# Kernel optimization log

Hardware: AMD Instinct MI355X
Metric: run time of the kernel (lower is better)

## Reference

```python
import jax, jax.numpy as jnp
import numpy as np

L, B, E = 512, 32, 512
ENC_HID, DEC_HID = 512, 1024
H2 = 2 * ENC_HID            # bidirectional encoder output dim
OUT_DIM = 32000             # generation (trg) vocab
CPY_LEN = 60000             # copy vocab size (embedding rows / prediction cols)
SRC_V = 50000
NEG = -1e10


def setup_inputs() -> dict:
    key = jax.random.key(0)
    ks = jax.random.split(key, 20)
    s = 0.02
    f32 = jnp.float32
    return {
        "src": jax.random.randint(ks[0], (L, B), 0, SRC_V),
        "inp": jax.random.randint(ks[1], (B,), 0, CPY_LEN),
        "hidden": jax.random.normal(ks[2], (2, B, DEC_HID), f32),
        "c": jax.random.normal(ks[3], (2, B, DEC_HID), f32),
        "encoder_outputs": jax.random.normal(ks[4], (L, B, H2), f32),
        "mask": jnp.ones((B, L), jnp.int32),
        "selective_weights": jax.random.normal(ks[5], (B, L - 2), f32),
        "src_to_cpy": jax.random.randint(ks[6], (SRC_V,), 0, CPY_LEN),
        # learned parameters
        "emb": jax.random.normal(ks[7], (CPY_LEN, E), f32) * s,
        "W_attn": jax.random.normal(ks[8], (H2 + DEC_HID, DEC_HID), f32) * s,
        "b_attn": jnp.zeros((DEC_HID,), f32),
        "v_attn": jax.random.normal(ks[9], (DEC_HID,), f32) * s,
        "W_ih0": jax.random.normal(ks[10], (4 * DEC_HID, 2 * H2 + E), f32) * s,
        "W_hh0": jax.random.normal(ks[11], (4 * DEC_HID, DEC_HID), f32) * s,
        "b_ih0": jnp.zeros((4 * DEC_HID,), f32),
        "b_hh0": jnp.zeros((4 * DEC_HID,), f32),
        "W_ih1": jax.random.normal(ks[12], (4 * DEC_HID, DEC_HID), f32) * s,
        "W_hh1": jax.random.normal(ks[13], (4 * DEC_HID, DEC_HID), f32) * s,
        "b_ih1": jnp.zeros((4 * DEC_HID,), f32),
        "b_hh1": jnp.zeros((4 * DEC_HID,), f32),
        "W_fc": jax.random.normal(ks[14], (OUT_DIM, H2 + DEC_HID + E), f32) * s,
        "b_fc": jnp.zeros((OUT_DIM,), f32),
        "W_copy": jax.random.normal(ks[15], (DEC_HID, H2), f32) * s,
        "b_copy": jnp.zeros((DEC_HID,), f32),
    }


def _lstm_cell(x, h, c, W_ih, W_hh, b_ih, b_hh):
    # PyTorch gate order: i, f, g, o
    g = x @ W_ih.T + h @ W_hh.T + b_ih + b_hh
    i, f, gg, o = jnp.split(g, 4, axis=-1)
    c_new = jax.nn.sigmoid(f) * c + jax.nn.sigmoid(i) * jnp.tanh(gg)
    h_new = jax.nn.sigmoid(o) * jnp.tanh(c_new)
    return h_new, c_new


def reference(src, inp, hidden, c, encoder_outputs, mask, selective_weights,
              src_to_cpy, emb, W_attn, b_attn, v_attn,
              W_ih0, W_hh0, b_ih0, b_hh0, W_ih1, W_hh1, b_ih1, b_hh1,
              W_fc, b_fc, W_copy, b_copy):
    Bn = encoder_outputs.shape[1]
    Ln = encoder_outputs.shape[0]
    # update_selective_weights: mask where converted src token != prev prediction, softmax
    conv_src = src_to_cpy[src[1:-1]]              # [L-2, B]
    copy_mask = (conv_src == inp[None, :]).T      # [B, L-2]
    sel = jnp.where(copy_mask, selective_weights, NEG)
    sel = jax.nn.softmax(sel, axis=1)             # [B, L-2]
    embedded = emb[inp]                           # [B, E] (dropout in eval mode = identity)
    enc = jnp.transpose(encoder_outputs, (1, 0, 2))  # [B, L, H2]
    # Bahdanau attention over encoder outputs
    h_top = hidden[-1]                            # [B, D]
    h_rep = jnp.broadcast_to(h_top[:, None, :], (Bn, Ln, h_top.shape[-1]))
    energy = jnp.tanh(jnp.concatenate([h_rep, enc], axis=2) @ W_attn + b_attn)  # [B, L, D]
    scores = energy @ v_attn                      # [B, L]
    scores = jnp.where(mask == 0, NEG, scores)
    attn_w = jax.nn.softmax(scores, axis=1)
    attentive_read = jnp.einsum('bl,blh->bh', attn_w, enc)        # [B, H2]
    sel = jnp.where(mask[:, 1:-1] == 0, NEG, sel)                 # faithful second mask
    selective_read = jnp.einsum('bl,blh->bh', sel, enc[:, 1:-1])  # [B, H2]
    # 2-layer LSTM, single step
    x = jnp.concatenate([embedded, attentive_read, selective_read], axis=1)
    h0, c0 = _lstm_cell(x, hidden[0], c[0], W_ih0, W_hh0, b_ih0, b_hh0)
    h1, c1 = _lstm_cell(h0, hidden[1], c[1], W_ih1, W_hh1, b_ih1, b_hh1)
    hidden_new = jnp.stack([h0, h1])
    c_new = jnp.stack([c0, c1])
    # generation scores
    gen = jnp.concatenate([h1, attentive_read, embedded], axis=1) @ W_fc.T + b_fc  # [B, OUT_DIM]
    # copy scores over trimmed source positions
    proj = jnp.tanh(enc[:, 1:-1] @ W_copy.T + b_copy)             # [B, L-2, D]
    copy_scores = jnp.einsum('bld,bd->bl', proj, h1)              # [B, L-2]
    copy_scores = jnp.where(mask[:, 1:-1] == 0, NEG, copy_scores)
    # assemble predictions: generation slice + indexed scatter of copy scores
    src_cpy = src_to_cpy[src.T[:, 1:-1]]                          # [B, L-2]
    preds = jnp.zeros((Bn, CPY_LEN), gen.dtype)
    preds = preds.at[:, :OUT_DIM].set(gen)
    preds = preds.at[jnp.arange(Bn)[:, None], src_cpy].set(copy_scores)
    return preds, hidden_new, c_new, attn_w, copy_scores
```

## Files before the change

### kernel.cpp

```cpp
#include <hip/hip_runtime.h>
#include <stdint.h>

typedef unsigned short u16;
typedef unsigned int   u32;
typedef __attribute__((ext_vector_type(8))) short short8;
typedef __attribute__((ext_vector_type(4))) float f32x4;

#define NEGF (-1.0e10f)

static constexpr int LL = 512, BB = 32, EE = 512, H2 = 1024, DH = 1024;
static constexpr int KX = 2560, OUTD = 32000, CPY = 60000;

static constexpr size_t HID_OFF   = 1920000;
static constexpr size_t C_OFF     = HID_OFF + 65536;
static constexpr size_t ATTN_OFF  = C_OFF + 65536;
static constexpr size_t CS_OFF    = ATTN_OFF + 16384;

static constexpr size_t WS_ENC    = 0;
static constexpr size_t WS_WA1T   = 33554432;
static constexpr size_t WS_WA2T   = 35651584;
static constexpr size_t WS_WCT    = 37748736;
static constexpr size_t WS_HPF    = 39845888;
static constexpr size_t WS_SCORES = 39976960;
static constexpr size_t WS_SELP   = 40108032;
static constexpr size_t WS_XBF    = 40173568;
static constexpr size_t WS_GENBF  = 40337408;
static constexpr size_t WS_H0PBF  = 40501248;
static constexpr size_t WS_H1PBF  = 40566784;
static constexpr size_t WS_H0NBF  = 40632320;
static constexpr size_t WS_PROJ   = 50331648;
static constexpr size_t WS_TOTAL  = WS_PROJ + 33554432;
static constexpr size_t WS_GPART  = WS_WA1T;
static constexpr size_t WS_TAG    = WS_ENC;

__device__ __forceinline__ u16 f2bf(float x){
  u32 u = __builtin_bit_cast(u32, x);
  u32 r = (u + 0x7FFFu + ((u >> 16) & 1u)) >> 16;
  return (u16)r;
}
__device__ __forceinline__ float bf2f(u16 h){
  u32 u = ((u32)h) << 16; return __builtin_bit_cast(float, u);
}
__device__ __forceinline__ float fsig(float x){ return 1.f/(1.f + __expf(-x)); }
__device__ __forceinline__ float ftanh(float x){
  float e = __expf(2.f*x);
  return 1.f - 2.f/(e + 1.f);
}

#define GLDS16(gp, lp) __builtin_amdgcn_global_load_lds( \
    (__attribute__((address_space(1))) void*)(gp), \
    (__attribute__((address_space(3))) void*)(lp), 16, 0, 0)

__global__ void k_f32_to_bf16(const float* __restrict__ in, u16* __restrict__ out, int n4){
  int stride = gridDim.x * blockDim.x;
  for (int i = blockIdx.x*blockDim.x + threadIdx.x; i < n4; i += stride){
    float4 v = ((const float4*)in)[i];
    u32 lo = (u32)f2bf(v.x) | ((u32)f2bf(v.y) << 16);
    u32 hi = (u32)f2bf(v.z) | ((u32)f2bf(v.w) << 16);
    ((uint2*)out)[i] = make_uint2(lo, hi);
  }
}

__global__ void k_wattn_t(const float* __restrict__ W, u16* __restrict__ wa1t, u16* __restrict__ wa2t){
  __shared__ float Tt[64*65];
  int n0 = blockIdx.x*64, k0 = blockIdx.y*64;
  int t = threadIdx.x;
  int nn = t & 63, kq = t >> 6;
  for (int kk = kq; kk < 64; kk += 4)
    Tt[kk*65 + nn] = W[(size_t)(k0+kk)*1024 + n0 + nn];
  __syncthreads();
  u16* dst = (k0 < 1024) ? wa1t : wa2t;
  int kbase = (k0 < 1024) ? k0 : (k0 - 1024);
  int kk2 = t & 63, nq = t >> 6;
  for (int nn2 = nq; nn2 < 64; nn2 += 4)
    dst[(size_t)(n0+nn2)*1024 + kbase + kk2] = f2bf(Tt[kk2*65 + nn2]);
}

__global__ void k_prep(const int* __restrict__ src, const int* __restrict__ inp,
                       const float* __restrict__ hidden, const float* __restrict__ selw,
                       const int* __restrict__ s2c, const float* __restrict__ emb,
                       const int* __restrict__ mask,
                       u16* __restrict__ xbf, u16* __restrict__ genbf,
                       u16* __restrict__ h0pbf, u16* __restrict__ h1pbf,
                       float* __restrict__ scores, float* __restrict__ selp)
{
  int b = blockIdx.x, t = threadIdx.x;
  int ib = inp[b];
  for (int h = t; h < 512; h += 256){
    u16 e = f2bf(emb[(size_t)ib*512 + h]);
    xbf[b*2560 + h] = e;
    genbf[b*2560 + 2048 + h] = e;
  }
  for (int k = t; k < 1024; k += 256){
    h0pbf[b*1024 + k] = f2bf(hidden[b*1024 + k]);
    h1pbf[b*1024 + k] = f2bf(hidden[32768 + b*1024 + k]);
  }
  for (int l = t; l < 512; l += 256)
    scores[b*512 + l] = 0.f;
  __shared__ float red[256];
  float lg[2];
  #pragma unroll
  for (int i = 0; i < 2; ++i){
    int j = t + i*256;
    lg[i] = NEGF;
    if (j < 510){
      int cs = s2c[src[(j+1)*32 + b]];
      if (cs == ib) lg[i] = selw[b*510 + j];
    }
  }
  red[t] = fmaxf(lg[0], lg[1]); __syncthreads();
  for (int s = 128; s > 0; s >>= 1){ if (t < s) red[t] = fmaxf(red[t], red[t+s]); __syncthreads(); }
  float mx = red[0]; __syncthreads();
  float e0 = (t < 510)     ? __expf(lg[0] - mx) : 0.f;
  float e1 = (t+256 < 510) ? __expf(lg[1] - mx) : 0.f;
  red[t] = e0 + e1; __syncthreads();
  for (int s = 128; s > 0; s >>= 1){ if (t < s) red[t] += red[t+s]; __syncthreads(); }
  float inv = 1.f / red[0];
  #pragma unroll
  for (int i = 0; i < 2; ++i){
    int j = t + i*256;
    if (j < 510){
      float v = ((i == 0) ? e0 : e1) * inv;
      int l = j + 1;
      selp[b*512 + l] = (mask[b*512 + l] != 0) ? v : NEGF;
    }
  }
}

__launch_bounds__(256)
__global__ void k_mfma(const u16* __restrict__ A, int lda, int Mvalid,
                       const u16* __restrict__ Bmat, int ldb, int K,
                       const float* __restrict__ preadd, int spa,
                       float* __restrict__ outstore, int NT)
{
  __shared__ u16 As[2][128*32];
  __shared__ u16 Bs[2][128*32];
  int wg = blockIdx.x;
  int mt = wg / NT, nt = wg % NT;
  int m0 = mt * 128, n0 = nt * 128;
  int tid = threadIdx.x, lane = tid & 63, wid = tid >> 6;
  int wm = wid >> 1, wn = wid & 1;

  f32x4 acc[4][4];
  #pragma unroll
  for (int i = 0; i < 4; ++i)
    #pragma unroll
    for (int j = 0; j < 4; ++j)
      acc[i][j] = (f32x4){0.f, 0.f, 0.f, 0.f};

  int r0 = tid >> 2,          s0 = tid & 3;
  int r1 = (tid + 256) >> 2;
  int xv0 = (r0 ^ (r0 >> 2)) & 3, xv1 = (r1 ^ (r1 >> 2)) & 3;
  int sc0 = (s0 ^ xv0) << 3,      sc1 = (s0 ^ xv1) << 3;
  int raA0 = m0 + r0; if (raA0 >= Mvalid) raA0 = Mvalid - 1;
  int raA1 = m0 + r1; if (raA1 >= Mvalid) raA1 = Mvalid - 1;
  int rbB0 = n0 + r0, rbB1 = n0 + r1;

  auto stage = [&](int k0, u16* asb, u16* bsb){
    GLDS16(A    + (size_t)raA0*lda + k0 + sc0, (char*)asb + tid*16);
    GLDS16(A    + (size_t)raA1*lda + k0 + sc1, (char*)asb + (tid+256)*16);
    GLDS16(Bmat + (size_t)rbB0*ldb + k0 + sc0, (char*)bsb + tid*16);
    GLDS16(Bmat + (size_t)rbB1*ldb + k0 + sc1, (char*)bsb + (tid+256)*16);
  };

  int KT = K >> 5;
  stage(0, As[0], Bs[0]);
  for (int kt = 0; kt < KT; ++kt){
    __syncthreads();
    if (kt + 1 < KT) stage((kt+1) << 5, As[(kt+1) & 1], Bs[(kt+1) & 1]);
    const char* ap = (const char*)As[kt & 1];
    const char* bp = (const char*)Bs[kt & 1];
    short8 af[4], bfr[4];
    #pragma unroll
    for (int mi = 0; mi < 4; ++mi){
      int rr = wm*64 + mi*16 + (lane & 15);
      int xv = (rr ^ (rr >> 2)) & 3;
      af[mi] = *(const short8*)(ap + rr*64 + (((lane >> 4) ^ xv) << 4));
    }
    #pragma unroll
    for (int nj = 0; nj < 4; ++nj){
      int rr = wn*64 + nj*16 + (lane & 15);
      int xv = (rr ^ (rr >> 2)) & 3;
      bfr[nj] = *(const short8*)(bp + rr*64 + (((lane >> 4) ^ xv) << 4));
    }
    #pragma unroll
    for (int mi = 0; mi < 4; ++mi)
      #pragma unroll
      for (int nj = 0; nj < 4; ++nj)
        acc[mi][nj] = __builtin_amdgcn_mfma_f32_16x16x32_bf16(af[mi], bfr[nj], acc[mi][nj], 0, 0, 0);
  }

  int g = lane >> 4, cn = lane & 15;
  int Nld = NT * 128;
  #pragma unroll
  for (int mi = 0; mi < 4; ++mi)
    #pragma unroll
    for (int rr2 = 0; rr2 < 4; ++rr2){
      int row = m0 + wm*64 + mi*16 + g*4 + rr2;
      if (row < Mvalid){
        #pragma unroll
        for (int nj = 0; nj < 4; ++nj){
          int n = n0 + wn*64 + nj*16 + cn;
          outstore[(size_t)row*Nld + n] = acc[mi][nj][rr2] + preadd[(size_t)(row & 31)*spa + n];
        }
      }
    }
}

__launch_bounds__(256, 2)
__global__ void k_mfma2(const u16* __restrict__ A, const u16* __restrict__ B1,
                        const u16* __restrict__ B2, const float* __restrict__ hpf,
                        const float* __restrict__ vattn, const float* __restrict__ bcopy,
                        float* __restrict__ scores, u16* __restrict__ projbf)
{
  __shared__ u16 As [2][128*32];
  __shared__ u16 B1s[2][128*32];
  __shared__ u16 B2s[2][128*32];
  const int lda = 1024;
  int nwg = gridDim.x, bid = blockIdx.x;
  int q = nwg >> 3, r = nwg & 7, xc = bid & 7, ix = bid >> 3;
  int wg = (xc < r ? xc*(q+1) : r*(q+1) + (xc - r)*q) + ix;
  int mt = wg >> 3, nt = wg & 7;
  int m0 = mt * 128, n0 = nt * 128;
  int tid = threadIdx.x, lane = tid & 63, wid = tid >> 6;
  int wm = wid >> 1, wn = wid & 1;

  f32x4 acc1[4][4], acc2[4][4];
  #pragma unroll
  for (int i = 0; i < 4; ++i)
    #pragma unroll
    for (int j = 0; j < 4; ++j){
      acc1[i][j] = (f32x4){0.f,0.f,0.f,0.f};
      acc2[i][j] = (f32x4){0.f,0.f,0.f,0.f};
    }

  int r0 = tid >> 2,          s0 = tid & 3;
  int r1 = (tid + 256) >> 2;
  int xv0 = (r0 ^ (r0 >> 2)) & 3, xv1 = (r1 ^ (r1 >> 2)) & 3;
  int sc0 = (s0 ^ xv0) << 3,      sc1 = (s0 ^ xv1) << 3;
  size_t a0 = (size_t)(m0 + r0)*lda, a1 = (size_t)(m0 + r1)*lda;
  size_t b0 = (size_t)(n0 + r0)*lda, b1o = (size_t)(n0 + r1)*lda;

  auto stage = [&](int k0, int buf){
    GLDS16(A  + a0  + k0 + sc0, (char*)As [buf] + tid*16);
    GLDS16(A  + a1  + k0 + sc1, (char*)As [buf] + (tid+256)*16);
    GLDS16(B1 + b0  + k0 + sc0, (char*)B1s[buf] + tid*16);
    GLDS16(B1 + b1o + k0 + sc1, (char*)B1s[buf] + (tid+256)*16);
    GLDS16(B2 + b0  + k0 + sc0, (char*)B2s[buf] + tid*16);
    GLDS16(B2 + b1o + k0 + sc1, (char*)B2s[buf] + (tid+256)*16);
  };

  stage(0, 0);
  for (int kt = 0; kt < 32; ++kt){
    __syncthreads();
    if (kt + 1 < 32) stage((kt+1) << 5, (kt+1) & 1);
    const char* ap  = (const char*)As [kt & 1];
    const char* b1p = (const char*)B1s[kt & 1];
    const char* b2p = (const char*)B2s[kt & 1];
    short8 af[4], bfr[4];
    #pragma unroll
    for (int mi = 0; mi < 4; ++mi){
      int rr = wm*64 + mi*16 + (lane & 15);
      int xv = (rr ^ (rr >> 2)) & 3;
      af[mi] = *(const short8*)(ap + rr*64 + (((lane >> 4) ^ xv) << 4));
    }
    #pragma unroll
    for (int nj = 0; nj < 4; ++nj){
      int rr = wn*64 + nj*16 + (lane & 15);
      int xv = (rr ^ (rr >> 2)) & 3;
      bfr[nj] = *(const short8*)(b1p + rr*64 + (((lane >> 4) ^ xv) << 4));
    }
    #pragma unroll
    for (int mi = 0; mi < 4; ++mi)
      #pragma unroll
      for (int nj = 0; nj < 4; ++nj)
        acc1[mi][nj] = __builtin_amdgcn_mfma_f32_16x16x32_bf16(af[mi], bfr[nj], acc1[mi][nj], 0, 0, 0);
    #pragma unroll
    for (int nj = 0; nj < 4; ++nj){
      int rr = wn*64 + nj*16 + (lane & 15);
      int xv = (rr ^ (rr >> 2)) & 3;
      bfr[nj] = *(const short8*)(b2p + rr*64 + (((lane >> 4) ^ xv) << 4));
    }
    #pragma unroll
    for (int mi = 0; mi < 4; ++mi)
      #pragma unroll
      for (int nj = 0; nj < 4; ++nj)
        acc2[mi][nj] = __builtin_amdgcn_mfma_f32_16x16x32_bf16(af[mi], bfr[nj], acc2[mi][nj], 0, 0, 0);
  }

  int g = lane >> 4, cn = lane & 15;
  #pragma unroll
  for (int mi = 0; mi < 4; ++mi)
    #pragma unroll
    for (int rr2 = 0; rr2 < 4; ++rr2){
      int row = m0 + wm*64 + mi*16 + g*4 + rr2;
      int bb = row & 31;
      float part = 0.f;
      #pragma unroll
      for (int nj = 0; nj < 4; ++nj){
        int n = n0 + wn*64 + nj*16 + cn;
        float tv = ftanh(acc1[mi][nj][rr2] + hpf[(size_t)bb*1024 + n]);
        part = fmaf(tv, vattn[n], part);
      }
      part += __shfl_xor(part, 1);
      part += __shfl_xor(part, 2);
      part += __shfl_xor(part, 4);
      part += __shfl_xor(part, 8);
      if (cn == 0) atomicAdd(&scores[(size_t)bb*512 + (row >> 5)], part);
    }
  #pragma unroll
  for (int mi = 0; mi < 4; ++mi)
    #pragma unroll
    for (int rr2 = 0; rr2 < 4; ++rr2){
      int row = m0 + wm*64 + mi*16 + g*4 + rr2;
      #pragma unroll
      for (int nj = 0; nj < 4; ++nj){
        int n = n0 + wn*64 + nj*16 + cn;
        projbf[(size_t)row*1024 + n] = f2bf(ftanh(acc2[mi][nj][rr2] + bcopy[n]));
      }
    }
}

__global__ void k_softmax_attn(const float* __restrict__ scores, const int* __restrict__ mask,
                               float* __restrict__ attnw){
  int b = blockIdx.x, t = threadIdx.x;
  __shared__ float red[256];
  float v0 = scores[b*512 + t];
  float v1 = scores[b*512 + 256 + t];
  if (mask[b*512 + t] == 0) v0 = NEGF;
  if (mask[b*512 + 256 + t] == 0) v1 = NEGF;
  red[t] = fmaxf(v0, v1); __syncthreads();
  for (int s = 128; s > 0; s >>= 1){ if (t < s) red[t] = fmaxf(red[t], red[t+s]); __syncthreads(); }
  float mx = red[0]; __syncthreads();
  float e0 = __expf(v0 - mx), e1 = __expf(v1 - mx);
  red[t] = e0 + e1; __syncthreads();
  for (int s = 128; s > 0; s >>= 1){ if (t < s) red[t] += red[t+s]; __syncthreads(); }
  float inv = 1.f / red[0];
  attnw[b*512 + t] = e0 * inv;
  attnw[b*512 + 256 + t] = e1 * inv;
}

__global__ void k_reads(const u16* __restrict__ encbf, const float* __restrict__ attnw,
                        const float* __restrict__ selp,
                        u16* __restrict__ xbf, u16* __restrict__ genbf){
  int b = blockIdx.y;
  int tid = threadIdx.x;
  int h = blockIdx.x*256 + (tid & 255);
  int lh = tid >> 8;
  float aa = 0.f, as = 0.f;
  int l0 = lh*256, l1 = l0 + 256;
  #pragma unroll 4
  for (int l = l0; l < l1; ++l){
    float e = bf2f(encbf[((size_t)l*32 + b)*1024 + h]);
    aa = fmaf(attnw[b*512 + l], e, aa);
    if (l >= 1 && l < 511) as = fmaf(selp[b*512 + l], e, as);
  }
  __shared__ float red[512][2];
  red[tid][0] = aa; red[tid][1] = as;
  __syncthreads();
  if (tid < 256){
    aa = red[tid][0] + red[tid+256][0];
    as = red[tid][1] + red[tid+256][1];
    u16 ab = f2bf(aa);
    xbf[b*2560 + 512 + h]    = ab;
    xbf[b*2560 + 1536 + h]   = f2bf(as);
    genbf[b*2560 + 1024 + h] = ab;
  }
}

__launch_bounds__(256)
__global__ void k_wgemm(const float* __restrict__ W1, const u16* __restrict__ xb1, int K1,
                        const float* __restrict__ W2, const u16* __restrict__ xb2, int K2,
                        const float* __restrict__ bias1, const float* __restrict__ bias2,
                        float* __restrict__ outB, int ldo, int cps)
{
  __shared__ u16 As[64*64];
  __shared__ u16 Bs[2][32*64];
  const int tid = threadIdx.x, lane = tid & 63, w = tid >> 6;
  const int o0 = blockIdx.x * 64;
  const int c1 = K1 >> 6;
  const int c0 = blockIdx.y * cps;

  f32x4 acc[2];
  acc[0] = (f32x4){0.f,0.f,0.f,0.f};
  acc[1] = (f32x4){0.f,0.f,0.f,0.f};

  const int ar = tid >> 2, akq = (tid & 3) * 16;
  const int aswz = (ar & 7) << 4;
  const int brow = tid >> 3, pslot = tid & 7;
  const int lslot = pslot ^ (brow & 7);

  float4 aA[4], aB[4];

  auto aload = [&](int c, float4* dst){
    const float* Wp; int Kp, kc;
    if (c < c1){ Wp = W1; Kp = K1; kc = c << 6; }
    else       { Wp = W2; Kp = K2; kc = (c - c1) << 6; }
    const float4* p = (const float4*)(Wp + (size_t)(o0 + ar)*Kp + kc + akq);
    dst[0] = p[0]; dst[1] = p[1]; dst[2] = p[2]; dst[3] = p[3];
  };
  auto bstage = [&](int c, u16* bsb){
    const u16* xp; int Kp, kc;
    if (c < c1){ xp = xb1; Kp = K1; kc = c << 6; }
    else       { xp = xb2; Kp = K2; kc = (c - c1) << 6; }
    GLDS16(xp + (size_t)brow*Kp + kc + lslot*8, (char*)bsb + tid*16);
  };

  auto body = [&](int c, float4* cur, float4* nxt, const u16* bsCur, u16* bsNxt, bool more){
    __syncthreads();
    if (more){ aload(c + 1, nxt); bstage(c + 1, bsNxt); }
    u32 p0 = (u32)f2bf(cur[0].x) | ((u32)f2bf(cur[0].y) << 16);
    u32 p1 = (u32)f2bf(cur[0].z) | ((u32)f2bf(cur[0].w) << 16);
    u32 p2 = (u32)f2bf(cur[1].x) | ((u32)f2bf(cur[1].y) << 16);
    u32 p3 = (u32)f2bf(cur[1].z) | ((u32)f2bf(cur[1].w) << 16);
    u32 p4 = (u32)f2bf(cur[2].x) | ((u32)f2bf(cur[2].y) << 16);
    u32 p5 = (u32)f2bf(cur[2].z) | ((u32)f2bf(cur[2].w) << 16);
    u32 p6 = (u32)f2bf(cur[3].x) | ((u32)f2bf(cur[3].y) << 16);
    u32 p7 = (u32)f2bf(cur[3].z) | ((u32)f2bf(cur[3].w) << 16);
    char* rowp = (char*)As + ar*128;
    *(uint4*)(rowp + ((akq*2)      ^ aswz)) = make_uint4(p0,p1,p2,p3);
    *(uint4*)(rowp + ((akq*2 + 16) ^ aswz)) = make_uint4(p4,p5,p6,p7);
    asm volatile("s_waitcnt lgkmcnt(0)" ::: "memory");
    __builtin_amdgcn_s_barrier();
    #pragma unroll
    for (int kk = 0; kk < 2; ++kk){
      int rrA = w*16 + (lane & 15);
      int kb  = kk*64 + ((lane >> 4) << 4);
      short8 af = *(const short8*)((const char*)As + rrA*128 + (kb ^ ((rrA & 7) << 4)));
      #pragma unroll
      for (int nj = 0; nj < 2; ++nj){
        int rrB = nj*16 + (lane & 15);
        short8 bfv = *(const short8*)((const char*)bsCur + rrB*128 + (kb ^ ((rrB & 7) << 4)));
        acc[nj] = __builtin_amdgcn_mfma_f32_16x16x32_bf16(af, bfv, acc[nj], 0, 0, 0);
      }
    }
  };

  aload(c0, aA); bstage(c0, Bs[0]);
  for (int li = 0; li < cps; li += 2){
    body(c0 + li,     aA, aB, Bs[0], Bs[1], true);
    body(c0 + li + 1, aB, aA, Bs[1], Bs[0], (li + 2) < cps);
  }

  int g = lane >> 4, cn = lane & 15;
  int ob = o0 + w*16 + g*4;
  float* outP = outB + (size_t)blockIdx.y * 32 * (size_t)ldo;
  float4 badd = make_float4(0.f,0.f,0.f,0.f);
  if (blockIdx.y == 0){
    if (bias1){ float4 t = *(const float4*)(bias1 + ob);
      badd.x += t.x; badd.y += t.y; badd.z += t.z; badd.w += t.w; }
    if (bias2){ float4 t = *(const float4*)(bias2 + ob);
      badd.x += t.x; badd.y += t.y; badd.z += t.z; badd.w += t.w; }
  }
  #pragma unroll
  for (int nj = 0; nj < 2; ++nj){
    int bcol = nj*16 + cn;
    float4 v = make_float4(acc[nj][0] + badd.x, acc[nj][1] + badd.y,
                           acc[nj][2] + badd.z, acc[nj][3] + badd.w);
    *(float4*)(outP + (size_t)bcol*ldo + ob) = v;
  }
}

__global__ void k_cell(const float* __restrict__ gpart, int nparts,
                       const float* __restrict__ c_in,
                       float* __restrict__ h_out, float* __restrict__ c_out,
                       u16* __restrict__ hbf, int hld){
  int idx = blockIdx.x*256 + threadIdx.x;
  int b = idx >> 10, j = idx & 1023;
  float gi = 0.f, gf = 0.f, gg = 0.f, go = 0.f;
  for (int p = 0; p < nparts; ++p){
    const float* gb = gpart + (size_t)p*131072 + (size_t)b*4096;
    gi += gb[j];
    gf += gb[1024 + j];
    gg += gb[2048 + j];
    go += gb[3072 + j];
  }
  float cv = c_in[b*1024 + j];
  float cnv = fsig(gf)*cv + fsig(gi)*ftanh(gg);
  float hn  = fsig(go)*ftanh(cnv);
  c_out[b*1024 + j] = cnv;
  h_out[b*1024 + j] = hn;
  hbf[(size_t)b*hld + j] = f2bf(hn);
}

__global__ void k_pdot(const u16* __restrict__ projbf, const u16* __restrict__ genbf,
                       const int* __restrict__ mask, const int* __restrict__ src,
                       const int* __restrict__ s2c,
                       float* __restrict__ cs_out, int* __restrict__ tag)
{
  int tid = threadIdx.x, lane = tid & 63, w = tid >> 6;
  int row = blockIdx.x*4 + w;
  int l = row >> 5, b = row & 31;
  const u16* pr = projbf + (size_t)row*1024 + lane*16;
  const u16* hr = genbf  + (size_t)b*2560 + lane*16;
  short8 p0 = *(const short8*)pr,     p1 = *(const short8*)(pr + 8);
  short8 h0 = *(const short8*)hr,     h1 = *(const short8*)(hr + 8);
  float s = 0.f;
  #pragma unroll
  for (int i = 0; i < 8; ++i) s = fmaf(bf2f((u16)p0[i]), bf2f((u16)h0[i]), s);
  #pragma unroll
  for (int i = 0; i < 8; ++i) s = fmaf(bf2f((u16)p1[i]), bf2f((u16)h1[i]), s);
  s += __shfl_xor(s, 1);  s += __shfl_xor(s, 2);  s += __shfl_xor(s, 4);
  s += __shfl_xor(s, 8);  s += __shfl_xor(s, 16); s += __shfl_xor(s, 32);
  if (lane == 0 && l >= 1 && l <= 510){
    int j = l - 1;
    cs_out[b*510 + j] = (mask[b*512 + l] != 0) ? s : NEGF;
    tag[(size_t)b*CPY + s2c[src[l*32 + b]]] = -1;
  }
}

__global__ void k_zerotail(float* __restrict__ preds){
  int i = blockIdx.x*256 + threadIdx.x;
  if (i < 224000){
    int b = i / 7000, t = i % 7000;
    ((float4*)(preds + (size_t)b*CPY + OUTD))[t] = make_float4(0.f, 0.f, 0.f, 0.f);
  }
}

__global__ void k_tag_max(const int* __restrict__ src, const int* __restrict__ s2c,
                          int* __restrict__ tag){
  int i = blockIdx.x*256 + threadIdx.x;
  if (i < 16320){
    int b = i / 510, j = i % 510;
    atomicMax(&tag[(size_t)b*CPY + s2c[src[(j+1)*32 + b]]], j);
  }
}
__global__ void k_tag_write(const int* __restrict__ src, const int* __restrict__ s2c,
                            const int* __restrict__ tag, const float* __restrict__ cs,
                            float* __restrict__ preds){
  int i = blockIdx.x*256 + threadIdx.x;
  if (i < 16320){
    int b = i / 510, j = i % 510;
    int idx = s2c[src[(j+1)*32 + b]];
    if (tag[(size_t)b*CPY + idx] == j)
      preds[(size_t)b*CPY + idx] = cs[b*510 + j];
  }
}

extern "C" void kernel_launch(void* const* d_in, const int* in_sizes, int n_in,
                              void* d_out, int out_size, void* d_ws, size_t ws_size,
                              hipStream_t stream){
  const int*   src    = (const int*)  d_in[0];
  const int*   inp    = (const int*)  d_in[1];
  const float* hidden = (const float*)d_in[2];
  const float* cst    = (const float*)d_in[3];
  const float* enc    = (const float*)d_in[4];
  const int*   mask   = (const int*)  d_in[5];
  const float* selw   = (const float*)d_in[6];
  const int*   s2c    = (const int*)  d_in[7];
  const float* emb    = (const float*)d_in[8];
  const float* W_attn = (const float*)d_in[9];
  const float* b_attn = (const float*)d_in[10];
  const float* v_attn = (const float*)d_in[11];
  const float* W_ih0  = (const float*)d_in[12];
  const float* W_hh0  = (const float*)d_in[13];
  const float* b_ih0  = (const float*)d_in[14];
  const float* b_hh0  = (const float*)d_in[15];
  const float* W_ih1  = (const float*)d_in[16];
  const float* W_hh1  = (const float*)d_in[17];
  const float* b_ih1  = (const float*)d_in[18];
  const float* b_hh1  = (const float*)d_in[19];
  const float* W_fc   = (const float*)d_in[20];
  const float* b_fc   = (const float*)d_in[21];
  const float* W_copy = (const float*)d_in[22];
  const float* b_copy = (const float*)d_in[23];

  if (ws_size < WS_TOTAL) return;

  float* out = (float*)d_out;
  char*  ws  = (char*)d_ws;
  u16*   encbf  = (u16*)  (ws + WS_ENC);
  u16*   wa1t   = (u16*)  (ws + WS_WA1T);
  u16*   wa2t   = (u16*)  (ws + WS_WA2T);
  u16*   wct    = (u16*)  (ws + WS_WCT);
  float* hpf    = (float*)(ws + WS_HPF);
  float* scores = (float*)(ws + WS_SCORES);
  float* selp   = (float*)(ws + WS_SELP);
  u16*   xbf    = (u16*)  (ws + WS_XBF);
  u16*   genbf  = (u16*)  (ws + WS_GENBF);
  u16*   h0pbf  = (u16*)  (ws + WS_H0PBF);
  u16*   h1pbf  = (u16*)  (ws + WS_H1PBF);
  u16*   h0nbf  = (u16*)  (ws + WS_H0NBF);
  u16*   projbf = (u16*)  (ws + WS_PROJ);
  float* gpart  = (float*)(ws + WS_GPART);
  int*   tag    = (int*)  (ws + WS_TAG);

  k_f32_to_bf16<<<2048, 256, 0, stream>>>(enc,    encbf, (LL*BB*H2)/4);
  k_f32_to_bf16<<<512,  256, 0, stream>>>(W_copy, wct,   (DH*H2)/4);
  k_wattn_t<<<dim3(16, 32), 256, 0, stream>>>(W_attn, wa1t, wa2t);
  k_prep<<<32, 256, 0, stream>>>(src, inp, hidden, selw, s2c, emb, mask,
                                 xbf, genbf, h0pbf, h1pbf, scores, selp);

  k_mfma<<<8, 256, 0, stream>>>(h1pbf, 1024, 32, wa1t, 1024, 1024,
                                b_attn, 0, hpf, 8);
  k_mfma2<<<1024, 256, 0, stream>>>(encbf, wa2t, wct, hpf, v_attn, b_copy,
                                    scores, projbf);
  k_softmax_attn<<<32, 256, 0, stream>>>(scores, mask, out + ATTN_OFF);
  k_reads<<<dim3(4, 32), 512, 0, stream>>>(encbf, out + ATTN_OFF, selp, xbf, genbf);

  k_wgemm<<<dim3(64, 7), 256, 0, stream>>>(W_ih0, xbf, KX, W_hh0, h0pbf, DH,
                                           b_ih0, b_hh0, gpart, 4096, 8);
  k_cell<<<128, 256, 0, stream>>>(gpart, 7, cst, out + HID_OFF, out + C_OFF,
                                  h0nbf, 1024);
  k_wgemm<<<dim3(64, 8), 256, 0, stream>>>(W_ih1, h0nbf, DH, W_hh1, h1pbf, DH,
                                           b_ih1, b_hh1, gpart, 4096, 4);
  k_cell<<<128, 256, 0, stream>>>(gpart, 8, cst + 32768, out + HID_OFF + 32768,
                                  out + C_OFF + 32768, genbf, 2560);

  k_pdot<<<4096, 256, 0, stream>>>(projbf, genbf, mask, src, s2c,
                                   out + CS_OFF, tag);

  k_wgemm<<<dim3(500, 1), 256, 0, stream>>>(W_fc, genbf, KX, nullptr, nullptr, 0,
                                            b_fc, nullptr, out, CPY, 40);
  k_zerotail<<<875, 256, 0, stream>>>(out);

  k_tag_max  <<<64, 256, 0, stream>>>(src, s2c, tag);
  k_tag_write<<<64, 256, 0, stream>>>(src, s2c, tag, out + CS_OFF, out);
}
```

Measured before the change: 378.8 us.

## Merge prep kernels into one launch and triple-buffer k_mfma2 loads

Four preprocessing kernels (enc/W_copy bf16 conversion, W_attn transpose, per-batch prep) and the tail-zeroing kernel become one block-dispatched kernel, removing several launches and letting the small tasks overlap with the large conversion. The fused attention/copy GEMM moves from a double-buffered LDS pipeline to a three-stage one. It uses explicit vmcnt waits and raw barriers so two k-tiles of global-to-LDS loads stay in flight. LDS use grows by half, which may lower occupancy under launch_bounds(256,2). The hand-written waitcnt relies on exactly six outstanding loads per stage.

```diff
diff --git a/kernel.cpp b/kernel.cpp
--- a/kernel.cpp
+++ b/kernel.cpp
@@ -51,78 +51,97 @@
     (__attribute__((address_space(1))) void*)(gp), \
     (__attribute__((address_space(3))) void*)(lp), 16, 0, 0)
 
-__global__ void k_f32_to_bf16(const float* __restrict__ in, u16* __restrict__ out, int n4){
-  int stride = gridDim.x * blockDim.x;
-  for (int i = blockIdx.x*blockDim.x + threadIdx.x; i < n4; i += stride){
-    float4 v = ((const float4*)in)[i];
-    u32 lo = (u32)f2bf(v.x) | ((u32)f2bf(v.y) << 16);
-    u32 hi = (u32)f2bf(v.z) | ((u32)f2bf(v.w) << 16);
-    ((uint2*)out)[i] = make_uint2(lo, hi);
-  }
-}
-
-__global__ void k_wattn_t(const float* __restrict__ W, u16* __restrict__ wa1t, u16* __restrict__ wa2t){
+__global__ void k_pre(const float* __restrict__ enc, u16* __restrict__ encbf,
+                      const float* __restrict__ W_copy, u16* __restrict__ wct,
+                      const float* __restrict__ W_attn, u16* __restrict__ wa1t, u16* __restrict__ wa2t,
+                      const int* __restrict__ src, const int* __restrict__ inp,
+                      const float* __restrict__ hidden, const float* __restrict__ selw,
+                      const int* __restrict__ s2c, const float* __restrict__ emb,
+                      const int* __restrict__ mask,
+                      u16* __restrict__ xbf, u16* __restrict__ genbf,
+                      u16* __restrict__ h0pbf, u16* __restrict__ h1pbf,
+                      float* __restrict__ scores, float* __restrict__ selp,
+                      float* __restrict__ preds)
+{
   __shared__ float Tt[64*65];
-  int n0 = blockIdx.x*64, k0 = blockIdx.y*64;
-  int t = threadIdx.x;
-  int nn = t & 63, kq = t >> 6;
-  for (int kk = kq; kk < 64; kk += 4)
-    Tt[kk*65 + nn] = W[(size_t)(k0+kk)*1024 + n0 + nn];
-  __syncthreads();
-  u16* dst = (k0 < 1024) ? wa1t : wa2t;
-  int kbase = (k0 < 1024) ? k0 : (k0 - 1024);
-  int kk2 = t & 63, nq = t >> 6;
-  for (int nn2 = nq; nn2 < 64; nn2 += 4)
-    dst[(size_t)(n0+nn2)*1024 + kbase + kk2] = f2bf(Tt[kk2*65 + nn2]);
-}
-
-__global__ void k_prep(const int* __restrict__ src, const int* __restrict__ inp,
-                       const float* __restrict__ hidden, const float* __restrict__ selw,
-                       const int* __restrict__ s2c, const float* __restrict__ emb,
-                       const int* __restrict__ mask,
-                       u16* __restrict__ xbf, u16* __restrict__ genbf,
-                       u16* __restrict__ h0pbf, u16* __restrict__ h1pbf,
-                       float* __restrict__ scores, float* __restrict__ selp)
-{
-  int b = blockIdx.x, t = threadIdx.x;
-  int ib = inp[b];
-  for (int h = t; h < 512; h += 256){
-    u16 e = f2bf(emb[(size_t)ib*512 + h]);
-    xbf[b*2560 + h] = e;
-    genbf[b*2560 + 2048 + h] = e;
-  }
-  for (int k = t; k < 1024; k += 256){
-    h0pbf[b*1024 + k] = f2bf(hidden[b*1024 + k]);
-    h1pbf[b*1024 + k] = f2bf(hidden[32768 + b*1024 + k]);
-  }
-  for (int l = t; l < 512; l += 256)
-    scores[b*512 + l] = 0.f;
   __shared__ float red[256];
-  float lg[2];
-  #pragma unroll
-  for (int i = 0; i < 2; ++i){
-    int j = t + i*256;
-    lg[i] = NEGF;
-    if (j < 510){
-      int cs = s2c[src[(j+1)*32 + b]];
-      if (cs == ib) lg[i] = selw[b*510 + j];
-    }
-  }
-  red[t] = fmaxf(lg[0], lg[1]); __syncthreads();
-  for (int s = 128; s > 0; s >>= 1){ if (t < s) red[t] = fmaxf(red[t], red[t+s]); __syncthreads(); }
-  float mx = red[0]; __syncthreads();
-  float e0 = (t < 510)     ? __expf(lg[0] - mx) : 0.f;
-  float e1 = (t+256 < 510) ? __expf(lg[1] - mx) : 0.f;
-  red[t] = e0 + e1; __syncthreads();
-  for (int s = 128; s > 0; s >>= 1){ if (t < s) red[t] += red[t+s]; __syncthreads(); }
-  float inv = 1.f / red[0];
-  #pragma unroll
-  for (int i = 0; i < 2; ++i){
-    int j = t + i*256;
-    if (j < 510){
-      float v = ((i == 0) ? e0 : e1) * inv;
-      int l = j + 1;
-      selp[b*512 + l] = (mask[b*512 + l] != 0) ? v : NEGF;
+  int bid = blockIdx.x, t = threadIdx.x;
+
+  if (bid < 1024){
+    int n4 = (LL*BB*H2)/4;
+    for (int i = bid*256 + t; i < n4; i += 1024*256){
+      float4 v = ((const float4*)enc)[i];
+      u32 lo = (u32)f2bf(v.x) | ((u32)f2bf(v.y) << 16);
+      u32 hi = (u32)f2bf(v.z) | ((u32)f2bf(v.w) << 16);
+      ((uint2*)encbf)[i] = make_uint2(lo, hi);
+    }
+  } else if (bid < 1152){
+    int i = (bid - 1024)*256 + t;
+    int n4 = (DH*H2)/4;
+    for (; i < n4; i += 128*256){
+      float4 v = ((const float4*)W_copy)[i];
+      u32 lo = (u32)f2bf(v.x) | ((u32)f2bf(v.y) << 16);
+      u32 hi = (u32)f2bf(v.z) | ((u32)f2bf(v.w) << 16);
+      ((uint2*)wct)[i] = make_uint2(lo, hi);
+    }
+  } else if (bid < 1664){
+    int idx = bid - 1152;
+    int n0 = (idx & 15)*64, k0 = (idx >> 4)*64;
+    int nn = t & 63, kq = t >> 6;
+    for (int kk = kq; kk < 64; kk += 4)
+      Tt[kk*65 + nn] = W_attn[(size_t)(k0+kk)*1024 + n0 + nn];
+    __syncthreads();
+    u16* dst = (k0 < 1024) ? wa1t : wa2t;
+    int kbase = (k0 < 1024) ? k0 : (k0 - 1024);
+    int kk2 = t & 63, nq = t >> 6;
+    for (int nn2 = nq; nn2 < 64; nn2 += 4)
+      dst[(size_t)(n0+nn2)*1024 + kbase + kk2] = f2bf(Tt[kk2*65 + nn2]);
+  } else if (bid < 1696){
+    int b = bid - 1664;
+    int ib = inp[b];
+    for (int h = t; h < 512; h += 256){
+      u16 e = f2bf(emb[(size_t)ib*512 + h]);
+      xbf[b*2560 + h] = e;
+      genbf[b*2560 + 2048 + h] = e;
+    }
+    for (int k = t; k < 1024; k += 256){
+      h0pbf[b*1024 + k] = f2bf(hidden[b*1024 + k]);
+      h1pbf[b*1024 + k] = f2bf(hidden[32768 + b*1024 + k]);
+    }
+    for (int l = t; l < 512; l += 256)
+      scores[b*512 + l] = 0.f;
+    float lg[2];
+    #pragma unroll
+    for (int i = 0; i < 2; ++i){
+      int j = t + i*256;
+      lg[i] = NEGF;
+      if (j < 510){
+        int cs = s2c[src[(j+1)*32 + b]];
+        if (cs == ib) lg[i] = selw[b*510 + j];
+      }
+    }
+    red[t] = fmaxf(lg[0], lg[1]); __syncthreads();
+    for (int s = 128; s > 0; s >>= 1){ if (t < s) red[t] = fmaxf(red[t], red[t+s]); __syncthreads(); }
+    float mx = red[0]; __syncthreads();
+    float e0 = (t < 510)     ? __expf(lg[0] - mx) : 0.f;
+    float e1 = (t+256 < 510) ? __expf(lg[1] - mx) : 0.f;
+    red[t] = e0 + e1; __syncthreads();
+    for (int s = 128; s > 0; s >>= 1){ if (t < s) red[t] += red[t+s]; __syncthreads(); }
+    float inv = 1.f / red[0];
+    #pragma unroll
+    for (int i = 0; i < 2; ++i){
+      int j = t + i*256;
+      if (j < 510){
+        float v = ((i == 0) ? e0 : e1) * inv;
+        int l = j + 1;
+        selp[b*512 + l] = (mask[b*512 + l] != 0) ? v : NEGF;
+      }
+    }
+  } else {
+    int i = (bid - 1696)*256 + t;
+    if (i < 224000){
+      int b = i / 7000, tt = i % 7000;
+      ((float4*)(preds + (size_t)b*CPY + OUTD))[tt] = make_float4(0.f,0.f,0.f,0.f);
     }
   }
 }
@@ -213,9 +232,9 @@
                         const float* __restrict__ vattn, const float* __restrict__ bcopy,
                         float* __restrict__ scores, u16* __restrict__ projbf)
 {
-  __shared__ u16 As [2][128*32];
-  __shared__ u16 B1s[2][128*32];
-  __shared__ u16 B2s[2][128*32];
+  __shared__ u16 As [3][128*32];
+  __shared__ u16 B1s[3][128*32];
+  __shared__ u16 B2s[3][128*32];
   const int lda = 1024;
   int nwg = gridDim.x, bid = blockIdx.x;
   int q = nwg >> 3, r = nwg & 7, xc = bid & 7, ix = bid >> 3;
@@ -241,7 +260,8 @@
   size_t a0 = (size_t)(m0 + r0)*lda, a1 = (size_t)(m0 + r1)*lda;
   size_t b0 = (size_t)(n0 + r0)*lda, b1o = (size_t)(n0 + r1)*lda;
 
-  auto stage = [&](int k0, int buf){
+  auto stage = [&](int kt, int buf){
+    int k0 = kt << 5;
     GLDS16(A  + a0  + k0 + sc0, (char*)As [buf] + tid*16);
     GLDS16(A  + a1  + k0 + sc1, (char*)As [buf] + (tid+256)*16);
     GLDS16(B1 + b0  + k0 + sc0, (char*)B1s[buf] + tid*16);
@@ -251,12 +271,17 @@
   };
 
   stage(0, 0);
+  stage(1, 1);
+  int cur = 0, pf = 2;
+  #pragma unroll 1
   for (int kt = 0; kt < 32; ++kt){
-    __syncthreads();
-    if (kt + 1 < 32) stage((kt+1) << 5, (kt+1) & 1);
-    const char* ap  = (const char*)As [kt & 1];
-    const char* b1p = (const char*)B1s[kt & 1];
-    const char* b2p = (const char*)B2s[kt & 1];
+    if (kt < 31) asm volatile("s_waitcnt vmcnt(6)" ::: "memory");
+    else         asm volatile("s_waitcnt vmcnt(0)" ::: "memory");
+    __builtin_amdgcn_s_barrier();
+    if (kt + 2 < 32) stage(kt + 2, pf);
+    const char* ap  = (const char*)As [cur];
+    const char* b1p = (const char*)B1s[cur];
+    const char* b2p = (const char*)B2s[cur];
     short8 af[4], bfr[4];
     #pragma unroll
     for (int mi = 0; mi < 4; ++mi){
@@ -286,6 +311,8 @@
       #pragma unroll
       for (int nj = 0; nj < 4; ++nj)
         acc2[mi][nj] = __builtin_amdgcn_mfma_f32_16x16x32_bf16(af[mi], bfr[nj], acc2[mi][nj], 0, 0, 0);
+    cur = (cur == 2) ? 0 : cur + 1;
+    pf  = (pf  == 2) ? 0 : pf  + 1;
   }
 
   int g = lane >> 4, cn = lane & 15;
@@ -506,14 +533,6 @@
     int j = l - 1;
     cs_out[b*510 + j] = (mask[b*512 + l] != 0) ? s : NEGF;
     tag[(size_t)b*CPY + s2c[src[l*32 + b]]] = -1;
-  }
-}
-
-__global__ void k_zerotail(float* __restrict__ preds){
-  int i = blockIdx.x*256 + threadIdx.x;
-  if (i < 224000){
-    int b = i / 7000, t = i % 7000;
-    ((float4*)(preds + (size_t)b*CPY + OUTD))[t] = make_float4(0.f, 0.f, 0.f, 0.f);
   }
 }
 
@@ -585,11 +604,9 @@
   float* gpart  = (float*)(ws + WS_GPART);
   int*   tag    = (int*)  (ws + WS_TAG);
 
-  k_f32_to_bf16<<<2048, 256, 0, stream>>>(enc,    encbf, (LL*BB*H2)/4);
-  k_f32_to_bf16<<<512,  256, 0, stream>>>(W_copy, wct,   (DH*H2)/4);
-  k_wattn_t<<<dim3(16, 32), 256, 0, stream>>>(W_attn, wa1t, wa2t);
-  k_prep<<<32, 256, 0, stream>>>(src, inp, hidden, selw, s2c, emb, mask,
-                                 xbf, genbf, h0pbf, h1pbf, scores, selp);
+  k_pre<<<2571, 256, 0, stream>>>(enc, encbf, W_copy, wct, W_attn, wa1t, wa2t,
+                                  src, inp, hidden, selw, s2c, emb, mask,
+                                  xbf, genbf, h0pbf, h1pbf, scores, selp, out);
 
   k_mfma<<<8, 256, 0, stream>>>(h1pbf, 1024, 32, wa1t, 1024, 1024,
                                 b_attn, 0, hpf, 8);
@@ -612,7 +629,6 @@
 
   k_wgemm<<<dim3(500, 1), 256, 0, stream>>>(W_fc, genbf, KX, nullptr, nullptr, 0,
                                             b_fc, nullptr, out, CPY, 40);
-  k_zerotail<<<875, 256, 0, stream>>>(out);
 
   k_tag_max  <<<64, 256, 0, stream>>>(src, s2c, tag);
   k_tag_write<<<64, 256, 0, stream>>>(src, s2c, tag, out + CS_OFF, out);
```

Result: faster. 355.0 us (-6.3%).
